# Kernel tuning notes

Measured on AMD Instinct MI355X. Metric: run time of the kernel, lower is better.

Reference implementation:

```python
import jax, jax.numpy as jnp
import numpy as np

N, E, C = 100000, 3200000, 30
IN, HID, OUT = 256, 256, 64


def _shapley_tables(max_n):
    # Closed form of the ShapleyGNNLayer per-node contribution:
    #   deg n == 0           : contrib = 0
    #   1 <= n <= 5 (exact)  : contrib = a(n)*x_i + b(n)*T_i,  a(n)=H_{n+1}/(n+1),
    #                          b(n) = -(H_{n+1}-1)/(n(n+1))   (H = harmonic number)
    #   n > 5 (Monte Carlo)  : permutation sum telescopes -> contrib = T_i/n exactly
    # where T_i = sum of neighbor features.
    H = np.concatenate([[0.0], np.cumsum(1.0 / np.arange(1, max_n + 2))])
    a = np.zeros(max_n + 1)
    b = np.zeros(max_n + 1)
    for m in range(1, max_n + 1):
        if m <= 5:
            a[m] = H[m + 1] / (m + 1)
            b[m] = -(H[m + 1] - 1.0) / (m * (m + 1))
        else:
            b[m] = 1.0 / m
    return jnp.asarray(a, jnp.float32), jnp.asarray(b, jnp.float32)


def _shapley_layer(x, mask, n_deg, a_tab, b_tab, W):
    T = mask @ x                                # [C,D] sum of neighbor feats
    a = a_tab[n_deg][:, None]
    b = b_tab[n_deg][:, None]
    sh = x + a * x + b * T                      # shapley_matrix (x[i] + contrib)
    return jax.nn.relu(sh @ W)


def setup_inputs() -> dict:
    key = jax.random.key(0)
    ks = jax.random.split(key, 10)
    s = 0.05
    return {
        "x": jax.random.normal(ks[0], (N, IN), jnp.float32),
        "edge_index": jax.random.randint(ks[1], (2, E), 0, N, dtype=jnp.int64)
        if jax.config.jax_enable_x64 else jax.random.randint(ks[1], (2, E), 0, N),
        "W_assign": jax.random.normal(ks[2], (IN, C), jnp.float32) * s,
        "b_assign": jnp.zeros((C,), jnp.float32),
        "W_proj": jax.random.normal(ks[3], (IN, IN), jnp.float32) * s,
        "b_proj": jnp.zeros((IN,), jnp.float32),
        "W_sh1": jax.random.normal(ks[4], (IN, HID), jnp.float32) * s,
        "W_sh2": jax.random.normal(ks[5], (HID, HID), jnp.float32) * s,
        "W_out": jax.random.normal(ks[6], (HID, OUT), jnp.float32) * s,
        "b_out": jnp.zeros((OUT,), jnp.float32),
    }


def reference(x, edge_index, W_assign, b_assign, W_proj, b_proj, W_sh1, W_sh2, W_out, b_out):
    n_nodes = x.shape[0]
    row, col = edge_index[0], edge_index[1]

    # --- MinCutPoolLayerSparse ---
    S = jax.nn.softmax(x @ W_assign + b_assign, axis=-1)        # [N,C]
    X_proj = x @ W_proj + b_proj                                 # [N,IN]
    Z = S.T @ X_proj                                             # [C,IN]
    adj_S = jax.ops.segment_sum(S[col], row, num_segments=n_nodes)   # A @ S, [N,C]
    adj_new = S.T @ adj_S                                        # [C,C]
    deg = jax.ops.segment_sum(jnp.ones((row.shape[0],), x.dtype), row,
                              num_segments=n_nodes)              # [N]
    vol = jnp.sum(S * deg[:, None])                              # trace(S^T D)
    cut = jnp.trace(adj_new)
    mincut_loss = -cut / (vol + 1e-9)
    SS = S.T @ S
    ortho_loss = jnp.linalg.norm(SS - jnp.eye(S.shape[1], dtype=S.dtype))

    # --- pooled edge structure (adj_pooled > 0) ---
    mask = (adj_new > 0).astype(x.dtype)                         # [C,C]
    n_deg = jnp.sum(adj_new > 0, axis=1)                         # [C] int
    a_tab, b_tab = _shapley_tables(S.shape[1])

    # --- Shapley GNN layers ---
    h = _shapley_layer(Z, mask, n_deg, a_tab, b_tab, W_sh1)
    h = _shapley_layer(h, mask, n_deg, a_tab, b_tab, W_sh2)
    out = h @ W_out + b_out
    return (out, mincut_loss, ortho_loss, Z, S)
```

## Files before the change

### kernel.cpp

```cpp
#include <hip/hip_runtime.h>
#include <math.h>

typedef float f32x4 __attribute__((ext_vector_type(4)));

#define N_NODES 100000
#define C_CL 30
#define D_IN 256

#define OUT_MAT 0
#define OUT_MC 1920
#define OUT_OR 1921
#define OUT_Z 1922
#define OUT_S 9602

#define WS_M 0
#define WS_SS 7680
#define WS_CS 8580
#define WS_CUT 8610
#define WS_H1 8640
#define WS_WT4 24000
#define WS_S8 32256
#define WS_SLAB0 835584

#define SLAB_SS2 7680
#define SLAB_CS2 8580
#define SLAB_STRIDE2 8640
#define MAX_R 512

#define CHUNK 128
#define NCHUNK ((N_NODES + CHUNK - 1) / CHUNK)

__global__ __launch_bounds__(256)
void k_prep(const float* __restrict__ Wa, float* __restrict__ ws) {
  const int b = blockIdx.x, t = threadIdx.x;
  if (b < 8) {
    const int g = b * 256 + t;
    const int k4 = g >> 5, c = g & 31;
    float4 v = make_float4(0.f, 0.f, 0.f, 0.f);
    if (c < C_CL) {
      v.x = Wa[(4 * k4 + 0) * C_CL + c];
      v.y = Wa[(4 * k4 + 1) * C_CL + c];
      v.z = Wa[(4 * k4 + 2) * C_CL + c];
      v.w = Wa[(4 * k4 + 3) * C_CL + c];
    }
    reinterpret_cast<float4*>(ws + WS_WT4)[g] = v;
  } else {
    if (t == 0) ws[WS_CUT] = 0.f;
  }
}

__global__ __launch_bounds__(256, 6)
void k_node(const float* __restrict__ x, const float* __restrict__ wt4f,
            const float* __restrict__ ba, float* __restrict__ S_out,
            unsigned* __restrict__ S8) {
  __shared__ float lg[64][33];
  const int t = threadIdx.x;
  const int lane = t & 63;
  const int cg = __builtin_amdgcn_readfirstlane(t >> 6);
  const int node = blockIdx.x * 64 + lane;
  const bool valid = (node < N_NODES);
  const int node_c = valid ? node : (N_NODES - 1);
  const f32x4* __restrict__ xr =
      reinterpret_cast<const f32x4*>(x) + (size_t)node_c * 64;
  const float4* __restrict__ wt4 = reinterpret_cast<const float4*>(wt4f);

  float acc[8];
  #pragma unroll
  for (int j = 0; j < 8; ++j) acc[j] = 0.f;

  #pragma unroll 8
  for (int k4 = 0; k4 < 64; ++k4) {
    const f32x4 xv = xr[k4];
    #pragma unroll
    for (int j = 0; j < 8; ++j) {
      const float4 wv = wt4[k4 * 32 + cg * 8 + j];
      acc[j] += xv.x * wv.x + xv.y * wv.y + xv.z * wv.z + xv.w * wv.w;
    }
  }
  #pragma unroll
  for (int j = 0; j < 8; ++j) lg[lane][cg * 8 + j] = acc[j];
  __syncthreads();

  if (t < 64) {
    if (valid) {
      float v[C_CL];
      float mx = -3.0e38f;
      #pragma unroll
      for (int c = 0; c < C_CL; ++c) {
        v[c] = lg[t][c] + ba[c];
        mx = fmaxf(mx, v[c]);
      }
      float sm = 0.f;
      #pragma unroll
      for (int c = 0; c < C_CL; ++c) { v[c] = __expf(v[c] - mx); sm += v[c]; }
      const float r = 1.f / sm;
      #pragma unroll
      for (int c = 0; c < C_CL; ++c) lg[t][c] = v[c] * r;
    } else {
      #pragma unroll
      for (int c = 0; c < C_CL; ++c) lg[t][c] = 0.f;
    }
    lg[t][30] = 0.f; lg[t][31] = 0.f;
  }
  __syncthreads();

  const int gbase = blockIdx.x * 1920;
  #pragma unroll
  for (int i = 0; i < 8; ++i) {
    const unsigned idx = i * 256 + t;
    if (idx < 1920u) {
      const unsigned n = idx / 30u, c = idx - 30u * n;
      const int g = gbase + (int)idx;
      if (g < N_NODES * C_CL) S_out[g] = lg[n][c];
    }
  }
  const unsigned sbase = (unsigned)blockIdx.x * 512;
  #pragma unroll
  for (int i = 0; i < 2; ++i) {
    const unsigned idx = i * 256 + t;
    const unsigned n = idx >> 3, j = idx & 7;
    const unsigned b0 = (unsigned)(lg[n][j * 4 + 0] * 255.f + 0.5f);
    const unsigned b1 = (unsigned)(lg[n][j * 4 + 1] * 255.f + 0.5f);
    const unsigned b2 = (unsigned)(lg[n][j * 4 + 2] * 255.f + 0.5f);
    const unsigned b3 = (unsigned)(lg[n][j * 4 + 3] * 255.f + 0.5f);
    S8[sbase + idx] = b0 | (b1 << 8) | (b2 << 16) | (b3 << 24);
  }
}

__device__ __forceinline__ int dd(unsigned a, unsigned b, int acc) {
  acc += (int)((a & 0xffu) * (b & 0xffu));
  acc += (int)(((a >> 8) & 0xffu) * ((b >> 8) & 0xffu));
  acc += (int)(((a >> 16) & 0xffu) * ((b >> 16) & 0xffu));
  acc += (int)((a >> 24) * (b >> 24));
  return acc;
}

__global__ __launch_bounds__(256)
void k_edges(const int* __restrict__ ei, const int E,
             const unsigned* __restrict__ S8, float* __restrict__ ws) {
  const int t = threadIdx.x;
  const int tid = blockIdx.x * 256 + t;
  const int* __restrict__ row = ei;
  const int* __restrict__ col = ei + E;
  float acc = 0.f;
  for (int e = tid; e < E; e += gridDim.x * 256) {
    const int r = row[e], c = col[e];
    const uint4* pr = reinterpret_cast<const uint4*>(S8 + (size_t)r * 8);
    const uint4* pc = reinterpret_cast<const uint4*>(S8 + (size_t)c * 8);
    const uint4 a0 = pr[0], a1 = pr[1];
    const uint4 b0 = pc[0], b1 = pc[1];
    int s = 0;
    s = dd(a0.x, b0.x, s); s = dd(a0.y, b0.y, s);
    s = dd(a0.z, b0.z, s); s = dd(a0.w, b0.w, s);
    s = dd(a1.x, b1.x, s); s = dd(a1.y, b1.y, s);
    s = dd(a1.z, b1.z, s); s = dd(a1.w, b1.w, s);
    acc += (float)s;
  }
  acc *= (1.f / 65025.f);
  #pragma unroll
  for (int m = 1; m < 64; m <<= 1) acc += __shfl_xor(acc, m, 64);
  __shared__ float wsum[4];
  if ((t & 63) == 0) wsum[t >> 6] = acc;
  __syncthreads();
  if (t == 0)
    atomicAdd(&ws[WS_CUT], wsum[0] + wsum[1] + wsum[2] + wsum[3]);
}

__global__ __launch_bounds__(256, 2)
void k_M2(const float* __restrict__ x, const float* __restrict__ Sp,
          float* __restrict__ slabs, const int R) {
  __shared__ float sraw[8192];
  float (*sm)[32] = reinterpret_cast<float (*)[32]>(sraw);
  const int t = threadIdx.x;
  const int h = t >> 7, sub = (t >> 6) & 1, lc = t & 63;
  const int i4 = (t >> 3) & 7, j4 = t & 7, w = t >> 6;
  const f32x4* __restrict__ x4 = reinterpret_cast<const f32x4*>(x);

  float a[16][4];
  #pragma unroll
  for (int j = 0; j < 16; ++j) { a[j][0] = 0.f; a[j][1] = 0.f; a[j][2] = 0.f; a[j][3] = 0.f; }
  float ssq[16];
  #pragma unroll
  for (int j = 0; j < 16; ++j) ssq[j] = 0.f;
  float cs = 0.f;

  for (int chunk = blockIdx.x; chunk < NCHUNK; chunk += R) {
    const int node0 = chunk * CHUNK;
    const int rows_valid = N_NODES - node0;
    __syncthreads();
    #pragma unroll
    for (int i = 0; i < 15; ++i) {
      const int idx = i * 256 + t;
      const int n = idx / 30, c = idx - 30 * n;
      const int g = node0 * C_CL + idx;
      sm[n][c] = (g < N_NODES * C_CL) ? Sp[g] : 0.f;
    }
    sm[t & 127][30 + (t >> 7)] = 0.f;
    __syncthreads();

    if (rows_valid >= CHUNK) {
      #pragma unroll 4
      for (int n = 0; n < 64; ++n) {
        const int nn = sub * 64 + n;
        const f32x4 xv = __builtin_nontemporal_load(&x4[(size_t)(node0 + nn) * 64 + lc]);
        const float4 s0 = *reinterpret_cast<const float4*>(&sm[nn][h * 16 + 0]);
        const float4 s1 = *reinterpret_cast<const float4*>(&sm[nn][h * 16 + 4]);
        const float4 s2 = *reinterpret_cast<const float4*>(&sm[nn][h * 16 + 8]);
        const float4 s3 = *reinterpret_cast<const float4*>(&sm[nn][h * 16 + 12]);
        const float sv[16] = {s0.x, s0.y, s0.z, s0.w, s1.x, s1.y, s1.z, s1.w,
                              s2.x, s2.y, s2.z, s2.w, s3.x, s3.y, s3.z, s3.w};
        #pragma unroll
        for (int j = 0; j < 16; ++j) {
          a[j][0] += sv[j] * xv.x; a[j][1] += sv[j] * xv.y;
          a[j][2] += sv[j] * xv.z; a[j][3] += sv[j] * xv.w;
        }
      }
    } else {
      for (int n = 0; n < 64; ++n) {
        const int nn = sub * 64 + n;
        f32x4 xv = (f32x4)0.f;
        if (nn < rows_valid) xv = x4[(size_t)(node0 + nn) * 64 + lc];
        const float4 s0 = *reinterpret_cast<const float4*>(&sm[nn][h * 16 + 0]);
        const float4 s1 = *reinterpret_cast<const float4*>(&sm[nn][h * 16 + 4]);
        const float4 s2 = *reinterpret_cast<const float4*>(&sm[nn][h * 16 + 8]);
        const float4 s3 = *reinterpret_cast<const float4*>(&sm[nn][h * 16 + 12]);
        const float sv[16] = {s0.x, s0.y, s0.z, s0.w, s1.x, s1.y, s1.z, s1.w,
                              s2.x, s2.y, s2.z, s2.w, s3.x, s3.y, s3.z, s3.w};
        #pragma unroll
        for (int j = 0; j < 16; ++j) {
          a[j][0] += sv[j] * xv.x; a[j][1] += sv[j] * xv.y;
          a[j][2] += sv[j] * xv.z; a[j][3] += sv[j] * xv.w;
        }
      }
    }

    #pragma unroll 4
    for (int n = 0; n < 32; ++n) {
      const int nn = w * 32 + n;
      const float4 av = *reinterpret_cast<const float4*>(&sm[nn][i4 * 4]);
      const float4 bv = *reinterpret_cast<const float4*>(&sm[nn][j4 * 4]);
      const float af[4] = {av.x, av.y, av.z, av.w};
      const float bf[4] = {bv.x, bv.y, bv.z, bv.w};
      #pragma unroll
      for (int ii = 0; ii < 4; ++ii)
        #pragma unroll
        for (int jj = 0; jj < 4; ++jj) ssq[ii * 4 + jj] += af[ii] * bf[jj];
    }
    if (t < C_CL) {
      #pragma unroll 4
      for (int n = 0; n < CHUNK; ++n) cs += sm[n][t];
    }
  }

  float* __restrict__ slab = slabs + (size_t)blockIdx.x * SLAB_STRIDE2;
  __syncthreads();
  if (sub == 1) {
    #pragma unroll
    for (int j = 0; j < 16; ++j) {
      const int c = h * 16 + j;
      if (c < C_CL) {
        #pragma unroll
        for (int q = 0; q < 4; ++q) sraw[c * 256 + lc * 4 + q] = a[j][q];
      }
    }
  }
  __syncthreads();
  if (sub == 0) {
    #pragma unroll
    for (int j = 0; j < 16; ++j) {
      const int c = h * 16 + j;
      if (c < C_CL) {
        #pragma unroll
        for (int q = 0; q < 4; ++q)
          slab[c * 256 + lc * 4 + q] = a[j][q] + sraw[c * 256 + lc * 4 + q];
      }
    }
  }
  __syncthreads();
  #pragma unroll
  for (int ii = 0; ii < 4; ++ii) {
    #pragma unroll
    for (int jj = 0; jj < 4; ++jj) {
      const int gi = i4 * 4 + ii, gj = j4 * 4 + jj;
      if (gi < C_CL && gj < C_CL)
        sraw[w * 900 + gi * C_CL + gj] = ssq[ii * 4 + jj];
    }
  }
  __syncthreads();
  for (int q = t; q < 900; q += 256)
    slab[SLAB_SS2 + q] = (sraw[q] + sraw[900 + q]) + (sraw[1800 + q] + sraw[2700 + q]);
  if (t < C_CL) slab[SLAB_CS2 + t] = cs;
}

__global__ __launch_bounds__(256)
void k_reduce(const float* __restrict__ slabs, const int R,
              float* __restrict__ ws) {
  const int i = blockIdx.x * 256 + threadIdx.x;
  if (i >= 8610) return;
  float s = 0.f;
  int r = 0;
  for (; r + 16 <= R; r += 16) {
    const float* p = slabs + (size_t)r * SLAB_STRIDE2 + i;
    float v[16];
    #pragma unroll
    for (int q = 0; q < 16; ++q) v[q] = p[(size_t)q * SLAB_STRIDE2];
    float s0 = ((v[0] + v[1]) + (v[2] + v[3])) + ((v[4] + v[5]) + (v[6] + v[7]));
    float s1 = ((v[8] + v[9]) + (v[10] + v[11])) + ((v[12] + v[13]) + (v[14] + v[15]));
    s += s0 + s1;
  }
  for (; r < R; ++r) s += slabs[(size_t)r * SLAB_STRIDE2 + i];
  ws[i] = s;
}

__global__ __launch_bounds__(256)
void k_z1(const float* __restrict__ ws, const float* __restrict__ Wp,
          const float* __restrict__ bp, const float* __restrict__ W1,
          float* __restrict__ out, float* __restrict__ h1out) {
  __shared__ float Mr[256], Mc[256], sh[256];
  const int r = blockIdx.x, t = threadIdx.x;
  float mc = 0.f;
  #pragma unroll
  for (int rr = 0; rr < C_CL; ++rr) mc += ws[WS_M + rr * 256 + t];
  Mc[t] = mc;
  Mr[t] = ws[WS_M + r * 256 + t];
  float scs = 0.f;
  #pragma unroll
  for (int rr = 0; rr < C_CL; ++rr) scs += ws[WS_CS + rr];
  __syncthreads();
  const float bpt = bp[t];
  float az = ws[WS_CS + r] * bpt;
  float ac = scs * bpt;
  #pragma unroll 8
  for (int k = 0; k < 256; ++k) {
    const float wv = Wp[(size_t)k * 256 + t];
    az += Mr[k] * wv;
    ac += Mc[k] * wv;
  }
  out[OUT_Z + r * 256 + t] = az;
  sh[t] = az + (1.f / 30.f) * ac;
  __syncthreads();
  float a1 = 0.f;
  #pragma unroll 8
  for (int k = 0; k < 256; ++k) a1 += sh[k] * W1[(size_t)k * 256 + t];
  h1out[r * 256 + t] = fmaxf(a1, 0.f);
}

__global__ __launch_bounds__(256)
void k_z2(const float* __restrict__ ws, const float* __restrict__ W2,
          const float* __restrict__ Wo, const float* __restrict__ bo,
          float* __restrict__ out, const float vol) {
  __shared__ float sh[256];
  __shared__ float h2[256];
  __shared__ float red[4][64];
  __shared__ float wsum[4];
  const int r = blockIdx.x, t = threadIdx.x;
  if (r < C_CL) {
    float cs1 = 0.f;
    #pragma unroll
    for (int rr = 0; rr < C_CL; ++rr) cs1 += ws[WS_H1 + rr * 256 + t];
    sh[t] = ws[WS_H1 + r * 256 + t] + (1.f / 30.f) * cs1;
    __syncthreads();
    float a2 = 0.f;
    #pragma unroll 8
    for (int k = 0; k < 256; ++k) a2 += sh[k] * W2[(size_t)k * 256 + t];
    h2[t] = fmaxf(a2, 0.f);
    __syncthreads();
    const int c = t & 63, q = t >> 6;
    float ao = 0.f;
    #pragma unroll 8
    for (int k = q * 64; k < q * 64 + 64; ++k) ao += h2[k] * Wo[k * 64 + c];
    red[q][c] = ao;
    __syncthreads();
    if (t < 64)
      out[OUT_MAT + r * 64 + t] =
          bo[t] + ((red[0][t] + red[1][t]) + (red[2][t] + red[3][t]));
  } else {
    float s = 0.f;
    for (int i = t; i < 900; i += 256) {
      const float d = ws[WS_SS + i] - ((i / C_CL == i % C_CL) ? 1.f : 0.f);
      s += d * d;
    }
    #pragma unroll
    for (int m = 1; m < 64; m <<= 1) s += __shfl_xor(s, m, 64);
    if ((t & 63) == 0) wsum[t >> 6] = s;
    __syncthreads();
    if (t == 0) {
      out[OUT_OR] = sqrtf(wsum[0] + wsum[1] + wsum[2] + wsum[3]);
      out[OUT_MC] = -ws[WS_CUT] / (vol + 1e-9f);
    }
  }
}

extern "C" void kernel_launch(void* const* d_in, const int* in_sizes, int n_in,
                              void* d_out, int out_size, void* d_ws, size_t ws_size,
                              hipStream_t stream) {
  (void)n_in; (void)out_size;
  const float* x  = (const float*)d_in[0];
  const int*   ei = (const int*)d_in[1];
  const float* Wa = (const float*)d_in[2];
  const float* ba = (const float*)d_in[3];
  const float* Wp = (const float*)d_in[4];
  const float* bp = (const float*)d_in[5];
  const float* W1 = (const float*)d_in[6];
  const float* W2 = (const float*)d_in[7];
  const float* Wo = (const float*)d_in[8];
  const float* bo = (const float*)d_in[9];
  float* out = (float*)d_out;
  float* ws  = (float*)d_ws;
  unsigned* S8 = (unsigned*)(ws + WS_S8);
  float* slabs = ws + WS_SLAB0;
  const int E = in_sizes[1] / 2;

  long avail = (long)(ws_size / 4) - WS_SLAB0;
  int R = (int)(avail / SLAB_STRIDE2);
  if (R > MAX_R) R = MAX_R;
  if (R < 1) R = 1;

  k_prep<<<9, 256, 0, stream>>>(Wa, ws);
  k_node<<<1563, 256, 0, stream>>>(x, ws + WS_WT4, ba, out + OUT_S, S8);
  k_edges<<<4096, 256, 0, stream>>>(ei, E, S8, ws);
  k_M2<<<R, 256, 0, stream>>>(x, out + OUT_S, slabs, R);
  k_reduce<<<34, 256, 0, stream>>>(slabs, R, ws);
  k_z1<<<C_CL, 256, 0, stream>>>(ws, Wp, bp, W1, out, ws + WS_H1);
  k_z2<<<C_CL + 1, 256, 0, stream>>>(ws, W2, Wo, bo, out, (float)E);
}
```

Before: 440.6 us.

## Stage node feature rows through swizzled double-buffered LDS in assignment kernel

The node kernel previously had each of the 4 wavefronts read the full 1KB x row per node directly from global memory, so the same row was fetched four times with strided, uncoalesced access. It now loads the 64x256 tile cooperatively with coalesced float4 loads into a double-buffered, XOR-swizzled shared buffer and computes from LDS. The next chunk is prefetched while the current one is consumed. This adds shared memory and two barriers per stage, so the occupancy hint is lowered from 6 to 4 blocks.

```diff
diff --git a/kernel.cpp b/kernel.cpp
--- a/kernel.cpp
+++ b/kernel.cpp
@@ -49,34 +49,63 @@
   }
 }
 
-__global__ __launch_bounds__(256, 6)
+__global__ __launch_bounds__(256, 4)
 void k_node(const float* __restrict__ x, const float* __restrict__ wt4f,
             const float* __restrict__ ba, float* __restrict__ S_out,
             unsigned* __restrict__ S8) {
   __shared__ float lg[64][33];
+  __shared__ float4 lx4[2][512];
   const int t = threadIdx.x;
   const int lane = t & 63;
   const int cg = __builtin_amdgcn_readfirstlane(t >> 6);
-  const int node = blockIdx.x * 64 + lane;
+  const int node0 = blockIdx.x * 64;
+  const int node = node0 + lane;
   const bool valid = (node < N_NODES);
-  const int node_c = valid ? node : (N_NODES - 1);
-  const f32x4* __restrict__ xr =
-      reinterpret_cast<const f32x4*>(x) + (size_t)node_c * 64;
   const float4* __restrict__ wt4 = reinterpret_cast<const float4*>(wt4f);
 
+  const int srow = t >> 3;
+  const int sch = t & 7;
+  const int ra = min(node0 + srow, N_NODES - 1);
+  const int rb = min(node0 + 32 + srow, N_NODES - 1);
+  const float* __restrict__ pa = x + (size_t)ra * 256 + sch * 4;
+  const float* __restrict__ pb = x + (size_t)rb * 256 + sch * 4;
+  const int wra = srow * 8 + (sch ^ (srow & 7));
+  const int wrb = wra + 256;
+  const int lsw3 = lane & 7;
+
   float acc[8];
   #pragma unroll
   for (int j = 0; j < 8; ++j) acc[j] = 0.f;
 
-  #pragma unroll 8
-  for (int k4 = 0; k4 < 64; ++k4) {
-    const f32x4 xv = xr[k4];
-    #pragma unroll
-    for (int j = 0; j < 8; ++j) {
-      const float4 wv = wt4[k4 * 32 + cg * 8 + j];
-      acc[j] += xv.x * wv.x + xv.y * wv.y + xv.z * wv.z + xv.w * wv.w;
-    }
-  }
+  float4 va = *reinterpret_cast<const float4*>(pa);
+  float4 vb = *reinterpret_cast<const float4*>(pb);
+  lx4[0][wra] = va;
+  lx4[0][wrb] = vb;
+  __syncthreads();
+
+  for (int s = 0; s < 8; ++s) {
+    if (s < 7) {
+      va = *reinterpret_cast<const float4*>(pa + (s + 1) * 32);
+      vb = *reinterpret_cast<const float4*>(pb + (s + 1) * 32);
+    }
+    const float4* __restrict__ lrow = &lx4[s & 1][lane * 8];
+    #pragma unroll
+    for (int c = 0; c < 8; ++c) {
+      const float4 xv = lrow[c ^ lsw3];
+      #pragma unroll
+      for (int j = 0; j < 8; ++j) {
+        const float4 wv = wt4[(s * 8 + c) * 32 + cg * 8 + j];
+        acc[j] += xv.x * wv.x + xv.y * wv.y + xv.z * wv.z + xv.w * wv.w;
+      }
+    }
+    if (s < 7) {
+      __syncthreads();
+      lx4[(s + 1) & 1][wra] = va;
+      lx4[(s + 1) & 1][wrb] = vb;
+      __syncthreads();
+    }
+  }
+
   #pragma unroll
   for (int j = 0; j < 8; ++j) lg[lane][cg * 8 + j] = acc[j];
   __syncthreads();
```

Result: faster. 421.5 us (-4.3%).
